# Kernel optimization log

Hardware: AMD Instinct MI355X
Metric: run time of the kernel (lower is better)

The kernel has to match this reference:

```python
import jax, jax.numpy as jnp
import numpy as np

NUM_TOKENS = 16384
DIM = 4096
N_EXPERTS = 256
ROUTE_SCALE = 1.0


def setup_inputs() -> dict:
    key = jax.random.key(0)
    k_x, k_w = jax.random.split(key)
    x = jax.random.normal(k_x, (NUM_TOKENS, DIM), dtype=jnp.float32)
    # nn.init.normal_(weight, std=0.02)
    weight = 0.02 * jax.random.normal(k_w, (N_EXPERTS, DIM), dtype=jnp.float32)
    return {"x": x, "weight": weight}


def reference(x, weight):
    # Router GEMM: [T, D] @ [D, E] -> [T, E]
    scores = jnp.einsum("td,ed->te", x, weight)
    # Eval-mode token_choice path: softmax in fp32
    probs = jax.nn.softmax(scores.astype(jnp.float32), axis=-1)  # [T, E]
    indices = jnp.argmax(probs, axis=-1, keepdims=True)  # [T, 1] int
    # Hard one-hot scatter of argmax
    y_hard = jax.nn.one_hot(indices[:, 0], N_EXPERTS, dtype=probs.dtype)  # [T, E]
    # Straight-through estimator mix
    ste = jax.lax.stop_gradient(y_hard - probs) + probs
    # Gather routing weight at the selected expert
    weights = jnp.take_along_axis(ste, indices, axis=-1)  # [T, 1]
    weights = (weights * ROUTE_SCALE).astype(x.dtype)
    return weights, indices
```

## Files before the change

kernel.cpp:

```cpp
#include <hip/hip_runtime.h>
#include <stdint.h>

#define NUM_TOKENS 16384
#define DIM        4096
#define NEXP       256
#define MB         64
#define BK         64
#define NITER      (DIM / BK)
#define APAD       72
#define NWAVES     16
#define MARGIN     0.025f
#define CAP        16384

typedef __attribute__((ext_vector_type(4))) float          f32x4;
typedef __attribute__((ext_vector_type(8))) __bf16         bf16x8;
typedef __attribute__((ext_vector_type(8))) unsigned short ushort8;

static __device__ __forceinline__ unsigned short f32_to_bf16(float f) {
    unsigned int u = __float_as_uint(f);
    u += 0x7fffu + ((u >> 16) & 1u);
    return (unsigned short)(u >> 16);
}

__global__ void cvt_weights(const float* __restrict__ w,
                            unsigned short* __restrict__ wh,
                            int* __restrict__ counter) {
    if (blockIdx.x == 0 && threadIdx.x == 0) *counter = 0;
    const int n8 = NEXP * DIM / 8;
    const int stride = gridDim.x * blockDim.x;
    for (int i = blockIdx.x * blockDim.x + threadIdx.x; i < n8; i += stride) {
        const int e  = i >> 9;
        const int k8 = i & 511;
        const int k  = k8 * 8;
        const int g    = e >> 4;
        const int col  = e & 15;
        const int it   = k8 >> 3;
        const int kk2  = (k8 >> 2) & 1;
        const int quad = k8 & 3;
        const int lane = quad * 16 + col;
        const int s    = ((g * 64 + it) * 2 + kk2) * 64 + lane;

        const float* src = w + (size_t)e * DIM + k;
        float4 v0 = *(const float4*)(src);
        float4 v1 = *(const float4*)(src + 4);
        ushort8 h;
        h[0] = f32_to_bf16(v0.x); h[1] = f32_to_bf16(v0.y);
        h[2] = f32_to_bf16(v0.z); h[3] = f32_to_bf16(v0.w);
        h[4] = f32_to_bf16(v1.x); h[5] = f32_to_bf16(v1.y);
        h[6] = f32_to_bf16(v1.z); h[7] = f32_to_bf16(v1.w);
        *(ushort8*)(wh + (size_t)s * 8) = h;
    }
}

__global__ __launch_bounds__(1024, 4) void gate_main(
    const float* __restrict__ x,
    const unsigned short* __restrict__ wh,
    float* __restrict__ out,
    int* __restrict__ counter,
    int4* __restrict__ entries)
{
    __shared__ unsigned short lAh[2][MB][APAD];
    __shared__ float4 cand[NWAVES][MB];

    const int tid  = threadIdx.x;
    const int wv   = tid >> 6;
    const int lane = tid & 63;
    const int tok0 = blockIdx.x * MB;

    const int ta   = tid >> 4;
    const int kcol = (tid & 15) * 4;
    const float* xrow = x + (size_t)(tok0 + ta) * DIM + kcol;

    const int quad = lane >> 4;
    const int col  = lane & 15;

    f32x4 acc[4];
    #pragma unroll
    for (int mt = 0; mt < 4; ++mt)
        acc[mt] = f32x4{0.f, 0.f, 0.f, 0.f};

    auto ldb = [&](int it, bf16x8 (&bc)[2]) {
        #pragma unroll
        for (int kk2 = 0; kk2 < 2; ++kk2)
            bc[kk2] = *(const bf16x8*)(wh +
                ((((size_t)wv * 64 + it) * 2 + kk2) * 64 + lane) * 8);
    };

    bf16x8 bA[2], bB[2];
    ldb(0, bA);
    ldb(1, bB);
    __builtin_amdgcn_sched_barrier(0);
    float4 x0  = *(const float4*)(xrow);
    float4 xva = *(const float4*)(xrow + 1 * BK);
    float4 xvb = *(const float4*)(xrow + 2 * BK);
    {
        ushort4 h;
        h.x = f32_to_bf16(x0.x); h.y = f32_to_bf16(x0.y);
        h.z = f32_to_bf16(x0.z); h.w = f32_to_bf16(x0.w);
        *(ushort4*)&lAh[0][ta][kcol] = h;
    }
    asm volatile("s_waitcnt lgkmcnt(0)" ::: "memory");
    __builtin_amdgcn_s_barrier();
    asm volatile("" ::: "memory");

    auto body = [&](int it, float4& xr, bf16x8 (&bc)[2]) {
        const int cur = it & 1;
        const int nxt = cur ^ 1;
        if (it + 1 < NITER) {
            ushort4 h;
            h.x = f32_to_bf16(xr.x); h.y = f32_to_bf16(xr.y);
            h.z = f32_to_bf16(xr.z); h.w = f32_to_bf16(xr.w);
            *(ushort4*)&lAh[nxt][ta][kcol] = h;
        }
        #pragma unroll
        for (int kk2 = 0; kk2 < 2; ++kk2) {
            bf16x8 ah[4];
            #pragma unroll
            for (int mt = 0; mt < 4; ++mt)
                ah[mt] = *(const bf16x8*)&lAh[cur][mt * 16 + col][kk2 * 32 + quad * 8];
            #pragma unroll
            for (int mt = 0; mt < 4; ++mt)
                acc[mt] = __builtin_amdgcn_mfma_f32_16x16x32_bf16(
                    ah[mt], bc[kk2], acc[mt], 0, 0, 0);
        }
        if (it + 2 < NITER)
            ldb(it + 2, bc);
        __builtin_amdgcn_sched_barrier(0);
        if (it + 3 < NITER)
            xr = *(const float4*)(xrow + (it + 3) * BK);
        asm volatile("s_waitcnt lgkmcnt(0)" ::: "memory");
        __builtin_amdgcn_s_barrier();
        asm volatile("" ::: "memory");
    };

    #pragma unroll 1
    for (int itb = 0; itb < NITER; itb += 2) {
        body(itb + 0, xva, bA);
        body(itb + 1, xvb, bB);
    }

    #pragma unroll
    for (int mt = 0; mt < 4; ++mt) {
        #pragma unroll
        for (int r = 0; r < 4; ++r) {
            float t1s = acc[mt][r]; int t1e = wv * 16 + col;
            float t2s = -__builtin_inff(); int t2e = 0x7fffffff;
            #pragma unroll
            for (int m = 1; m <= 8; m <<= 1) {
                float o1s = __shfl_xor(t1s, m); int o1e = __shfl_xor(t1e, m);
                float o2s = __shfl_xor(t2s, m); int o2e = __shfl_xor(t2e, m);
                bool o1_top = (o1s > t1s) || (o1s == t1s && o1e < t1e);
                if (o1_top) {
                    bool keep_t1 = (t1s > o2s) || (t1s == o2s && t1e < o2e);
                    t2s = keep_t1 ? t1s : o2s; t2e = keep_t1 ? t1e : o2e;
                    t1s = o1s; t1e = o1e;
                } else {
                    bool o1_2nd = (o1s > t2s) || (o1s == t2s && o1e < t2e);
                    if (o1_2nd) { t2s = o1s; t2e = o1e; }
                }
            }
            if (col == 0) {
                int tok = mt * 16 + quad * 4 + r;
                cand[wv][tok] = make_float4(t1s, __int_as_float(t1e), t2s, __int_as_float(t2e));
            }
        }
    }
    __syncthreads();

    if (tid < MB) {
        float4 c0 = cand[0][tid];
        float t1s = c0.x; int t1e = __float_as_int(c0.y);
        float t2s = c0.z; int t2e = __float_as_int(c0.w);
        #pragma unroll
        for (int wvi = 1; wvi < NWAVES; ++wvi) {
            float4 c = cand[wvi][tid];
            float o1s = c.x; int o1e = __float_as_int(c.y);
            float o2s = c.z; int o2e = __float_as_int(c.w);
            bool o1_top = (o1s > t1s) || (o1s == t1s && o1e < t1e);
            if (o1_top) {
                bool keep_t1 = (t1s > o2s) || (t1s == o2s && t1e < o2e);
                t2s = keep_t1 ? t1s : o2s; t2e = keep_t1 ? t1e : o2e;
                t1s = o1s; t1e = o1e;
            } else {
                bool o1_2nd = (o1s > t2s) || (o1s == t2s && o1e < t2e);
                if (o1_2nd) { t2s = o1s; t2e = o1e; }
            }
        }
        const int gtok = tok0 + tid;
        out[gtok] = 1.0f;
        out[NUM_TOKENS + gtok] = (float)t1e;
        if (t1s - t2s < MARGIN) {
            int slot = atomicAdd(counter, 1);
            if (slot < CAP) entries[slot] = make_int4(gtok, t1e, t2e, 0);
        }
    }
}

__global__ void refine(const float* __restrict__ x,
                       const float* __restrict__ w,
                       const int* __restrict__ counter,
                       const int4* __restrict__ entries,
                       float* __restrict__ out) {
    const int gwave  = (blockIdx.x * blockDim.x + threadIdx.x) >> 6;
    const int lane   = threadIdx.x & 63;
    const int nwaves = (gridDim.x * blockDim.x) >> 6;
    int n = *counter; if (n > CAP) n = CAP;
    for (int i = gwave; i < n; i += nwaves) {
        int4 e = entries[i];
        const float* xr = x + (size_t)e.x * DIM;
        const float* w1 = w + (size_t)e.y * DIM;
        const float* w2 = w + (size_t)e.z * DIM;
        double d1 = 0.0, d2 = 0.0;
        for (int k = lane; k < DIM; k += 64) {
            double xv = (double)xr[k];
            d1 += xv * (double)w1[k];
            d2 += xv * (double)w2[k];
        }
        #pragma unroll
        for (int m = 32; m > 0; m >>= 1) {
            d1 += __shfl_xor(d1, m);
            d2 += __shfl_xor(d2, m);
        }
        if (lane == 0) {
            int best = (d1 > d2) ? e.y : ((d2 > d1) ? e.z : (e.y < e.z ? e.y : e.z));
            out[NUM_TOKENS + e.x] = (float)best;
        }
    }
}

extern "C" void kernel_launch(void* const* d_in, const int* in_sizes, int n_in,
                              void* d_out, int out_size, void* d_ws, size_t ws_size,
                              hipStream_t stream) {
    const float* x = (const float*)d_in[0];
    const float* w = (const float*)d_in[1];
    float* out = (float*)d_out;

    char* ws = (char*)d_ws;
    unsigned short* wh = (unsigned short*)ws;
    int*  counter = (int*)(ws + (2u << 20));
    int4* entries = (int4*)(ws + (2u << 20) + 16);

    cvt_weights<<<256, 256, 0, stream>>>(w, wh, counter);
    gate_main<<<NUM_TOKENS / MB, 1024, 0, stream>>>(x, wh, out, counter, entries);
    refine<<<256, 256, 0, stream>>>(x, w, counter, entries, out);
}
```

Before: 435.5 us.

## Retile router GEMM to 2x2 wave tiles with BK=256 and fewer barriers

Raises the K step from 64 to 256 so each block hits a barrier 16 times instead of 64. Each wave now computes a 32-token by 32-expert tile (2x2 MFMAs) instead of 64x16, which reuses both A and B fragments. The weight layout is flattened into 32-wide K chunks, and those B fragments are software-prefetched per inner step. The top-2 reduction is adjusted to 8 expert groups. The larger LDS tile (about 67KB) and wider x loads may lower occupancy and raise register pressure.

```diff
diff --git a/kernel.cpp b/kernel.cpp
--- a/kernel.cpp
+++ b/kernel.cpp
@@ -5,9 +5,10 @@
 #define DIM        4096
 #define NEXP       256
 #define MB         64
-#define BK         64
+#define BK         256
 #define NITER      (DIM / BK)
-#define APAD       72
+#define NKK        (BK / 32)
+#define AROW       264
 #define NWAVES     16
 #define MARGIN     0.025f
 #define CAP        16384
@@ -34,11 +35,10 @@
         const int k  = k8 * 8;
         const int g    = e >> 4;
         const int col  = e & 15;
-        const int it   = k8 >> 3;
-        const int kk2  = (k8 >> 2) & 1;
+        const int c    = k8 >> 2;
         const int quad = k8 & 3;
         const int lane = quad * 16 + col;
-        const int s    = ((g * 64 + it) * 2 + kk2) * 64 + lane;
+        const int s    = (g * 128 + c) * 64 + lane;
 
         const float* src = w + (size_t)e * DIM + k;
         float4 v0 = *(const float4*)(src);
@@ -59,92 +59,108 @@
     int* __restrict__ counter,
     int4* __restrict__ entries)
 {
-    __shared__ unsigned short lAh[2][MB][APAD];
-    __shared__ float4 cand[NWAVES][MB];
+    __shared__ unsigned short lAh[2][MB][AROW];
+    __shared__ float4 cand[8][MB];
 
     const int tid  = threadIdx.x;
     const int wv   = tid >> 6;
     const int lane = tid & 63;
     const int tok0 = blockIdx.x * MB;
 
+    const int th  = wv & 1;
+    const int ewv = wv >> 1;
+
     const int ta   = tid >> 4;
-    const int kcol = (tid & 15) * 4;
-    const float* xrow = x + (size_t)(tok0 + ta) * DIM + kcol;
+    const int kc16 = (tid & 15) * 16;
+    const float* xrow = x + (size_t)(tok0 + ta) * DIM + kc16;
 
     const int quad = lane >> 4;
     const int col  = lane & 15;
 
-    f32x4 acc[4];
+    f32x4 acc[2][2];
     #pragma unroll
-    for (int mt = 0; mt < 4; ++mt)
-        acc[mt] = f32x4{0.f, 0.f, 0.f, 0.f};
-
-    auto ldb = [&](int it, bf16x8 (&bc)[2]) {
-        #pragma unroll
-        for (int kk2 = 0; kk2 < 2; ++kk2)
-            bc[kk2] = *(const bf16x8*)(wh +
-                ((((size_t)wv * 64 + it) * 2 + kk2) * 64 + lane) * 8);
+    for (int mt = 0; mt < 2; ++mt)
+        #pragma unroll
+        for (int nt = 0; nt < 2; ++nt)
+            acc[mt][nt] = f32x4{0.f, 0.f, 0.f, 0.f};
+
+    auto ldb = [&](int c, bf16x8 (&bc)[2]) {
+        #pragma unroll
+        for (int nt = 0; nt < 2; ++nt)
+            bc[nt] = *(const bf16x8*)(wh +
+                (((size_t)(ewv * 2 + nt) * 128 + c) * 64 + lane) * 8);
     };
 
+    struct XQ { float4 a, b, c, d; };
+    auto ldx = [&](int it) {
+        XQ v;
+        const float* p = xrow + it * BK;
+        v.a = *(const float4*)(p);
+        v.b = *(const float4*)(p + 4);
+        v.c = *(const float4*)(p + 8);
+        v.d = *(const float4*)(p + 12);
+        return v;
+    };
+    auto stageA = [&](int slot, const XQ& v) {
+        ushort8 h0, h1;
+        h0[0] = f32_to_bf16(v.a.x); h0[1] = f32_to_bf16(v.a.y);
+        h0[2] = f32_to_bf16(v.a.z); h0[3] = f32_to_bf16(v.a.w);
+        h0[4] = f32_to_bf16(v.b.x); h0[5] = f32_to_bf16(v.b.y);
+        h0[6] = f32_to_bf16(v.b.z); h0[7] = f32_to_bf16(v.b.w);
+        h1[0] = f32_to_bf16(v.c.x); h1[1] = f32_to_bf16(v.c.y);
+        h1[2] = f32_to_bf16(v.c.z); h1[3] = f32_to_bf16(v.c.w);
+        h1[4] = f32_to_bf16(v.d.x); h1[5] = f32_to_bf16(v.d.y);
+        h1[6] = f32_to_bf16(v.d.z); h1[7] = f32_to_bf16(v.d.w);
+        *(ushort8*)&lAh[slot][ta][kc16]     = h0;
+        *(ushort8*)&lAh[slot][ta][kc16 + 8] = h1;
+    };
+
+    XQ xq = ldx(0);
+    stageA(0, xq);
+    xq = ldx(1);
     bf16x8 bA[2], bB[2];
     ldb(0, bA);
-    ldb(1, bB);
-    __builtin_amdgcn_sched_barrier(0);
-    float4 x0  = *(const float4*)(xrow);
-    float4 xva = *(const float4*)(xrow + 1 * BK);
-    float4 xvb = *(const float4*)(xrow + 2 * BK);
-    {
-        ushort4 h;
-        h.x = f32_to_bf16(x0.x); h.y = f32_to_bf16(x0.y);
-        h.z = f32_to_bf16(x0.z); h.w = f32_to_bf16(x0.w);
-        *(ushort4*)&lAh[0][ta][kcol] = h;
-    }
     asm volatile("s_waitcnt lgkmcnt(0)" ::: "memory");
     __builtin_amdgcn_s_barrier();
-    asm volatile("" ::: "memory");
-
-    auto body = [&](int it, float4& xr, bf16x8 (&bc)[2]) {
+    __builtin_amdgcn_sched_barrier(0);
+
+    #pragma unroll 1
+    for (int it = 0; it < NITER; ++it) {
         const int cur = it & 1;
         const int nxt = cur ^ 1;
         if (it + 1 < NITER) {
-            ushort4 h;
-            h.x = f32_to_bf16(xr.x); h.y = f32_to_bf16(xr.y);
-            h.z = f32_to_bf16(xr.z); h.w = f32_to_bf16(xr.w);
-            *(ushort4*)&lAh[nxt][ta][kcol] = h;
-        }
-        #pragma unroll
-        for (int kk2 = 0; kk2 < 2; ++kk2) {
-            bf16x8 ah[4];
-            #pragma unroll
-            for (int mt = 0; mt < 4; ++mt)
-                ah[mt] = *(const bf16x8*)&lAh[cur][mt * 16 + col][kk2 * 32 + quad * 8];
-            #pragma unroll
-            for (int mt = 0; mt < 4; ++mt)
-                acc[mt] = __builtin_amdgcn_mfma_f32_16x16x32_bf16(
-                    ah[mt], bc[kk2], acc[mt], 0, 0, 0);
-        }
-        if (it + 2 < NITER)
-            ldb(it + 2, bc);
-        __builtin_amdgcn_sched_barrier(0);
-        if (it + 3 < NITER)
-            xr = *(const float4*)(xrow + (it + 3) * BK);
+            stageA(nxt, xq);
+            if (it + 2 < NITER)
+                xq = ldx(it + 2);
+        }
+        #pragma unroll
+        for (int kk = 0; kk < NKK; ++kk) {
+            bf16x8 (&bc)[2] = (kk & 1) ? bB : bA;
+            bf16x8 (&bn)[2] = (kk & 1) ? bA : bB;
+            const int c = it * NKK + kk;
+            if (c + 1 < DIM / 32)
+                ldb(c + 1, bn);
+            bf16x8 ah0 = *(const bf16x8*)&lAh[cur][th * 32 + col][kk * 32 + quad * 8];
+            bf16x8 ah1 = *(const bf16x8*)&lAh[cur][th * 32 + 16 + col][kk * 32 + quad * 8];
+            acc[0][0] = __builtin_amdgcn_mfma_f32_16x16x32_bf16(ah0, bc[0], acc[0][0], 0, 0, 0);
+            acc[1][0] = __builtin_amdgcn_mfma_f32_16x16x32_bf16(ah1, bc[0], acc[1][0], 0, 0, 0);
+            acc[0][1] = __builtin_amdgcn_mfma_f32_16x16x32_bf16(ah0, bc[1], acc[0][1], 0, 0, 0);
+            acc[1][1] = __builtin_amdgcn_mfma_f32_16x16x32_bf16(ah1, bc[1], acc[1][1], 0, 0, 0);
+        }
         asm volatile("s_waitcnt lgkmcnt(0)" ::: "memory");
         __builtin_amdgcn_s_barrier();
-        asm volatile("" ::: "memory");
-    };
-
-    #pragma unroll 1
-    for (int itb = 0; itb < NITER; itb += 2) {
-        body(itb + 0, xva, bA);
-        body(itb + 1, xvb, bB);
+        __builtin_amdgcn_sched_barrier(0);
     }
 
     #pragma unroll
-    for (int mt = 0; mt < 4; ++mt) {
+    for (int mt = 0; mt < 2; ++mt) {
         #pragma unroll
         for (int r = 0; r < 4; ++r) {
-            float t1s = acc[mt][r]; int t1e = wv * 16 + col;
-            float t2s = -__builtin_inff(); int t2e = 0x7fffffff;
+            float s0 = acc[mt][0][r]; int e0 = ewv * 32 + col;
+            float s1 = acc[mt][1][r]; int e1 = e0 + 16;
+            float t1s, t2s; int t1e, t2e;
+            if (s1 > s0) { t1s = s1; t1e = e1; t2s = s0; t2e = e0; }
+            else         { t1s = s0; t1e = e0; t2s = s1; t2e = e1; }
             #pragma unroll
             for (int m = 1; m <= 8; m <<= 1) {
                 float o1s = __shfl_xor(t1s, m); int o1e = __shfl_xor(t1e, m);
@@ -160,8 +176,8 @@
                 }
             }
             if (col == 0) {
-                int tok = mt * 16 + quad * 4 + r;
-                cand[wv][tok] = make_float4(t1s, __int_as_float(t1e), t2s, __int_as_float(t2e));
+                int tok = th * 32 + mt * 16 + quad * 4 + r;
+                cand[ewv][tok] = make_float4(t1s, __int_as_float(t1e), t2s, __int_as_float(t2e));
             }
         }
     }
@@ -172,8 +188,8 @@
         float t1s = c0.x; int t1e = __float_as_int(c0.y);
         float t2s = c0.z; int t2e = __float_as_int(c0.w);
         #pragma unroll
-        for (int wvi = 1; wvi < NWAVES; ++wvi) {
-            float4 c = cand[wvi][tid];
+        for (int e = 1; e < 8; ++e) {
+            float4 c = cand[e][tid];
             float o1s = c.x; int o1e = __float_as_int(c.y);
             float o2s = c.z; int o2e = __float_as_int(c.w);
             bool o1_top = (o1s > t1s) || (o1s == t1s && o1e < t1e);
```

Measured after the change: 430.4 us. Within noise of the previous version (-1.2%).
